# Performance work log

Hardware: AMD Instinct MI355X
Metric: run time of the kernel (lower is better)

## Reference

```python
import jax, jax.numpy as jnp
import numpy as np

B, N_IN, N_HID, N_OUT = 1024, 1024, 2048, 32000


def setup_inputs() -> dict:
    key = jax.random.key(0)
    ks = jax.random.split(key, 9)
    s = lambda fan_in: 1.0 / np.sqrt(fan_in)
    return {
        "input": jax.random.normal(ks[0], (B, N_IN), jnp.float32),
        "hidden": jax.random.normal(ks[1], (B, N_HID), jnp.float32),
        "W_i2g": jax.random.normal(ks[2], (2 * N_HID, N_IN + N_HID), jnp.float32) * s(N_IN + N_HID),
        "b_i2g": jax.random.normal(ks[3], (2 * N_HID,), jnp.float32) * s(N_IN + N_HID),
        "W_x2h": jax.random.normal(ks[4], (N_HID, N_IN), jnp.float32) * s(N_IN),
        "b_x2h": jax.random.normal(ks[5], (N_HID,), jnp.float32) * s(N_IN),
        "W_h2h": jax.random.normal(ks[6], (N_HID, N_HID), jnp.float32) * s(N_HID),
        "W_h2o": jax.random.normal(ks[7], (N_OUT, N_HID), jnp.float32) * s(N_HID),
        "b_h2o": jax.random.normal(ks[8], (N_OUT,), jnp.float32) * s(N_HID),
    }


def reference(input, hidden, W_i2g, b_i2g, W_x2h, b_x2h, W_h2h, W_h2o, b_h2o):
    # combined = cat([input, hidden], dim=1); gates = sigmoid(i2g(combined))
    combined = jnp.concatenate([input, hidden], axis=1)           # [B, n_in+n_hid]
    gates = jax.nn.sigmoid(combined @ W_i2g.T + b_i2g)            # [B, 2*n_hid]
    z, r = gates[:, :N_HID], gates[:, N_HID:]
    # candidate h: tanh(x2h(x) + h2h(r*h)); GRU blend
    h_cand = jnp.tanh(input @ W_x2h.T + b_x2h + (r * hidden) @ W_h2h.T)
    h = z * hidden + (1.0 - z) * h_cand                           # [B, n_hid]
    # dropout in eval mode = identity; h2o + log_softmax over dim 1
    logits = h @ W_h2o.T + b_h2o                                  # [B, n_out]
    output = jax.nn.log_softmax(logits, axis=1)
    return (output, h)
```

## Files before the change

kernel.cpp:

```cpp
#include <hip/hip_runtime.h>
#include <hip/hip_bf16.h>
#include <stdint.h>

using bf16 = __hip_bfloat16;
typedef __bf16 bf16x8 __attribute__((ext_vector_type(8)));
typedef float f32x4 __attribute__((ext_vector_type(4)));

__device__ __forceinline__ void gload_lds16(const bf16* g, bf16* l) {
  __builtin_amdgcn_global_load_lds(
      (const __attribute__((address_space(1))) void*)g,
      (__attribute__((address_space(3))) void*)l, 16, 0, 0);
}

#define BARRIER() asm volatile("s_barrier" ::: "memory")

struct CvtArgs {
  const float* src[5];
  bf16* dst[5];
  int n[5];
  int bstart[6];
};

__global__ __launch_bounds__(256) void cvt_all(CvtArgs a) {
  int seg = 0;
#pragma unroll
  for (int i = 0; i < 4; ++i)
    if ((int)blockIdx.x >= a.bstart[i + 1]) seg = i + 1;
  const int nb = a.bstart[seg + 1] - a.bstart[seg];
  const int lb = blockIdx.x - a.bstart[seg];
  const float* __restrict__ in = a.src[seg];
  bf16* __restrict__ out = a.dst[seg];
  const int n = a.n[seg];
  const int stride = nb * 256 * 4;
  for (int i = (lb * 256 + (int)threadIdx.x) * 4; i < n; i += stride) {
    float4 v = *reinterpret_cast<const float4*>(in + i);
    union { bf16 h[4]; uint2 u; } o;
    o.h[0] = __float2bfloat16(v.x);
    o.h[1] = __float2bfloat16(v.y);
    o.h[2] = __float2bfloat16(v.z);
    o.h[3] = __float2bfloat16(v.w);
    *reinterpret_cast<uint2*>(out + i) = o.u;
  }
}

template <int EPI>
__global__ __launch_bounds__(256)
void gemm128(const bf16* __restrict__ A0, const bf16* __restrict__ A1,
             int aSplit, int ldA0, int ldA1,
             const bf16* __restrict__ B0, const bf16* __restrict__ B1,
             int bSplit, int ldB0, int ldB1,
             int MB, int N, int K,
             const float* __restrict__ bias,
             const float* __restrict__ hidden,
             const bf16* __restrict__ zbuf,
             bf16* __restrict__ obf_a,
             bf16* __restrict__ obf_b,
             float* __restrict__ of32,
             int gemmBlocks,
             const float* __restrict__ csrc,
             bf16* __restrict__ cdst, int cn) {
  const int tid = threadIdx.x;
  if ((int)blockIdx.x >= gemmBlocks) {
    const int cb = blockIdx.x - gemmBlocks;
    const int ncb = gridDim.x - gemmBlocks;
    const int stride = ncb * 256 * 4;
    for (int i = (cb * 256 + tid) * 4; i < cn; i += stride) {
      float4 v = *reinterpret_cast<const float4*>(csrc + i);
      union { bf16 h[4]; uint2 u; } o;
      o.h[0] = __float2bfloat16(v.x);
      o.h[1] = __float2bfloat16(v.y);
      o.h[2] = __float2bfloat16(v.z);
      o.h[3] = __float2bfloat16(v.w);
      *reinterpret_cast<uint2*>(cdst + i) = o.u;
    }
    return;
  }
  __shared__ bf16 lA[2][128 * 64];
  __shared__ bf16 lB[2][128 * 64];
  const int wave = tid >> 6;
  const int lane = tid & 63;
  const int cpx = gemmBlocks >> 3;
  const int swz = ((int)blockIdx.x & 7) * cpx + ((int)blockIdx.x >> 3);
  const int bm = swz % MB;
  const int bn = swz / MB;
  const int wr = wave >> 1, wc = wave & 1;
  const int l8 = lane >> 3;
  const int gcol = ((lane & 7) ^ l8) * 8;
  const int lrow = lane & 15;
  const int kb0 = (lane >> 4) * 16;
  const int xm = (lane & 7) << 4;
  const int nkt = K >> 6;

  auto STAGEK = [&](int buf, int kt) {
    if (kt >= nkt) return;
    const int kb = kt << 6;
    const bf16* Ap; int lda, ka;
    if (kb < aSplit) { Ap = A0; lda = ldA0; ka = kb; }
    else             { Ap = A1; lda = ldA1; ka = kb - aSplit; }
    const bf16* Bp; int ldb, kbb;
    if (kb < bSplit) { Bp = B0; ldb = ldB0; kbb = kb; }
    else             { Bp = B1; ldb = ldB1; kbb = kb - bSplit; }
#pragma unroll
    for (int h = 0; h < 2; ++h)
#pragma unroll
      for (int j = 0; j < 2; ++j) {
        const int r0 = h * 64 + wave * 16 + j * 8;
        gload_lds16(Ap + (size_t)(bm * 128 + r0 + l8) * lda + ka + gcol,
                    &lA[buf][r0 * 64]);
        gload_lds16(Bp + (size_t)(bn * 128 + r0 + l8) * ldb + kbb + gcol,
                    &lB[buf][r0 * 64]);
      }
  };
  auto RDA = [&](int buf, int row, int ks) {
    return *reinterpret_cast<const bf16x8*>(
        reinterpret_cast<const char*>(&lA[buf][0]) + row * 128 +
        ((ks * 64 + kb0) ^ xm));
  };
  auto RDB = [&](int buf, int row, int ks) {
    return *reinterpret_cast<const bf16x8*>(
        reinterpret_cast<const char*>(&lB[buf][0]) + row * 128 +
        ((ks * 64 + kb0) ^ xm));
  };

  f32x4 acc[4][4] = {};

  STAGEK(0, 0);
  asm volatile("s_waitcnt vmcnt(0)" ::: "memory");
  BARRIER();

  for (int kt = 0; kt < nkt; ++kt) {
    const int buf = kt & 1;
    STAGEK(buf ^ 1, kt + 1);
    bf16x8 af[4][2], bfr[4][2];
#pragma unroll
    for (int f = 0; f < 4; ++f)
#pragma unroll
      for (int ks = 0; ks < 2; ++ks) {
        af[f][ks] = RDA(buf, wr * 64 + f * 16 + lrow, ks);
        bfr[f][ks] = RDB(buf, wc * 64 + f * 16 + lrow, ks);
      }
    __builtin_amdgcn_s_setprio(1);
#pragma unroll
    for (int fm = 0; fm < 4; ++fm)
#pragma unroll
      for (int fn = 0; fn < 4; ++fn)
#pragma unroll
        for (int ks = 0; ks < 2; ++ks)
          acc[fm][fn] = __builtin_amdgcn_mfma_f32_16x16x32_bf16(
              af[fm][ks], bfr[fn][ks], acc[fm][fn], 0, 0, 0);
    __builtin_amdgcn_s_setprio(0);
    asm volatile("s_waitcnt vmcnt(0)" ::: "memory");
    BARRIER();
  }

  const int rb = bm * 128 + wr * 64 + (lane >> 4) * 4;
  const int cb = bn * 128 + wc * 64 + lrow;
#pragma unroll
  for (int fm = 0; fm < 4; ++fm) {
#pragma unroll
    for (int fn = 0; fn < 4; ++fn) {
#pragma unroll
      for (int j = 0; j < 4; ++j) {
        const int m = rb + fm * 16 + j;
        const int n = cb + fn * 16;
        float v = acc[fm][fn][j];
        if (EPI == 1) {
          v = 1.0f / (1.0f + __expf(-(v + bias[n])));
          if (n < 2048) {
            obf_a[(size_t)m * 2048 + n] = __float2bfloat16(v);
          } else {
            const int nn = n - 2048;
            obf_b[(size_t)m * 2048 + nn] =
                __float2bfloat16(v * hidden[(size_t)m * 2048 + nn]);
          }
        } else if (EPI == 2) {
          const float e = __expf(2.0f * (v + bias[n]));
          const float hc = (e - 1.0f) / (e + 1.0f);
          const float z = __bfloat162float(zbuf[(size_t)m * 2048 + n]);
          const float hd = hidden[(size_t)m * 2048 + n];
          const float h = z * hd + (1.0f - z) * hc;
          of32[(size_t)m * 2048 + n] = h;
          obf_a[(size_t)m * 2048 + n] = __float2bfloat16(h);
        }
      }
    }
  }
}

__global__ __launch_bounds__(512, 2)
void gemm256_f(const bf16* __restrict__ A, const bf16* __restrict__ W,
               const float* __restrict__ bias, uint32_t* __restrict__ lgt,
               float2* __restrict__ partials, int MB, int K, int NPB) {
  __shared__ bf16 lds[5][256 * 64];
  const int tid = threadIdx.x;
  const int w = tid >> 6, lane = tid & 63;
  const int nwg = gridDim.x;
  const int q8 = nwg >> 3, r8 = nwg & 7;
  const int xcd = (int)blockIdx.x & 7, lid = (int)blockIdx.x >> 3;
  const int swz =
      (xcd < r8 ? xcd * (q8 + 1) : r8 * (q8 + 1) + (xcd - r8) * q8) + lid;
  const int bm = swz % MB, bn = swz / MB;
  const int wr = w >> 2, wc = w & 3;
  const int l8 = lane >> 3;
  const int gcol = ((lane & 7) ^ l8) * 8;
  const int rA = lane & 15;
  const int kb0 = (lane >> 4) * 16;
  const int xm = (lane & 7) << 4;
  const int nkt = K >> 6, niter = nkt >> 1;
  const bf16* gA = A + (size_t)bm * 256 * K;
  const bf16* gB = W + (size_t)bn * 256 * K;

  auto STAGE2 = [&](int plane, int kt, const bf16* g) {
    if (kt > nkt - 1) kt = nkt - 1;
#pragma unroll
    for (int h = 0; h < 2; ++h) {
      const int r0 = h * 128 + w * 16;
#pragma unroll
      for (int j = 0; j < 2; ++j)
        gload_lds16(g + (size_t)(r0 + j * 8 + l8) * K + kt * 64 + gcol,
                    &lds[plane][(r0 + j * 8) * 64]);
    }
  };
  auto RD = [&](int plane, int row, int ks) {
    const int off = row * 128 + ((ks * 64 + kb0) ^ xm);
    return *reinterpret_cast<const bf16x8*>(
        reinterpret_cast<const char*>(&lds[plane][0]) + off);
  };

  f32x4 acc[8][4] = {};

  int a0 = 0, a1 = 1, a2 = 2;
  STAGE2(a0, 0, gA); STAGE2(3, 0, gB);
  STAGE2(a1, 1, gA); STAGE2(4, 1, gB);
  asm volatile("s_waitcnt vmcnt(8)" ::: "memory");
  BARRIER();

  for (int it = 0; it < niter; ++it) {
    const int t = it << 1;
    const bool last = (it == niter - 1);
    bf16x8 bfr[4][2];
#pragma unroll
    for (int ph = 0; ph < 8; ++ph) {
      const int buf = ph >> 2, q = ph & 3;
      const int ap = buf ? a1 : a0;
      const int bp = 3 + buf;
      bf16x8 af[2][2];
      if (q == 0) {
#pragma unroll
        for (int n = 0; n < 4; ++n)
#pragma unroll
          for (int ks = 0; ks < 2; ++ks)
            bfr[n][ks] = RD(bp, wc * 64 + n * 16 + rA, ks);
      }
#pragma unroll
      for (int mm = 0; mm < 2; ++mm)
#pragma unroll
        for (int ks = 0; ks < 2; ++ks)
          af[mm][ks] = RD(ap, wr * 128 + (q * 2 + mm) * 16 + rA, ks);

      if (ph == 1)      STAGE2(a2, t + 2, gA);
      else if (ph == 2) STAGE2(3, t + 2, gB);
      else if (ph == 5) STAGE2(a0, t + 3, gA);
      else if (ph == 6) STAGE2(4, t + 3, gB);

      if (ph == 3 || ph == 7)
        asm volatile("s_waitcnt vmcnt(8)" ::: "memory");
      if (!(ph == 7 && last)) BARRIER();
      __builtin_amdgcn_sched_barrier(0);

      __builtin_amdgcn_s_setprio(1);
#pragma unroll
      for (int mm = 0; mm < 2; ++mm)
#pragma unroll
        for (int n = 0; n < 4; ++n)
#pragma unroll
          for (int ks = 0; ks < 2; ++ks)
            acc[q * 2 + mm][n] = __builtin_amdgcn_mfma_f32_16x16x32_bf16(
                af[mm][ks], bfr[n][ks], acc[q * 2 + mm][n], 0, 0, 0);
      __builtin_amdgcn_s_setprio(0);
    }
    const int na0 = a2, na1 = a0, na2 = a1;
    a0 = na0; a1 = na1; a2 = na2;
  }
  asm volatile("s_waitcnt vmcnt(0) lgkmcnt(0)" ::: "memory");
  __syncthreads();

  float* red = (float*)&lds[0][0];
  float* red2 = red + 1024;
  const int outc = bn * 256 + wc * 64 + rA;
  float bb[4];
#pragma unroll
  for (int n = 0; n < 4; ++n) bb[n] = bias[outc + n * 16];
#pragma unroll
  for (int m = 0; m < 8; ++m)
#pragma unroll
    for (int n = 0; n < 4; ++n)
#pragma unroll
      for (int j = 0; j < 4; ++j) acc[m][n][j] += bb[n];

  const int q4 = lane >> 4;
  const int rowb = wr * 128 + q4 * 4;
#pragma unroll
  for (int m = 0; m < 8; ++m)
#pragma unroll
    for (int j = 0; j < 4; ++j) {
      float x = fmaxf(fmaxf(acc[m][0][j], acc[m][1][j]),
                      fmaxf(acc[m][2][j], acc[m][3][j]));
      x = fmaxf(x, __shfl_xor(x, 1));
      x = fmaxf(x, __shfl_xor(x, 2));
      x = fmaxf(x, __shfl_xor(x, 4));
      x = fmaxf(x, __shfl_xor(x, 8));
      if (rA == 0) red[wc * 256 + rowb + m * 16 + j] = x;
    }
  __syncthreads();
  if (tid < 256)
    red2[tid] = fmaxf(fmaxf(red[0 * 256 + tid], red[1 * 256 + tid]),
                      fmaxf(red[2 * 256 + tid], red[3 * 256 + tid]));
  __syncthreads();

  uint32_t* lgtb = lgt + (size_t)(bm * NPB + bn) * (64 * 512) + tid;
#pragma unroll
  for (int m = 0; m < 8; ++m) {
    const int r0 = rowb + m * 16;
    float s[4];
#pragma unroll
    for (int j = 0; j < 4; ++j) {
      const float fm = red2[r0 + j];
      float e = __expf(acc[m][0][j] - fm) + __expf(acc[m][1][j] - fm) +
                __expf(acc[m][2][j] - fm) + __expf(acc[m][3][j] - fm);
      e += __shfl_xor(e, 1);
      e += __shfl_xor(e, 2);
      e += __shfl_xor(e, 4);
      e += __shfl_xor(e, 8);
      s[j] = e;
    }
#pragma unroll
    for (int j = 0; j < 4; ++j)
      if (rA == 0) red[wc * 256 + r0 + j] = s[j];
#pragma unroll
    for (int n = 0; n < 4; ++n)
#pragma unroll
      for (int k = 0; k < 2; ++k) {
        union { bf16 h[2]; uint32_t u; } pk;
        pk.h[0] = __float2bfloat16(acc[m][n][2 * k]);
        pk.h[1] = __float2bfloat16(acc[m][n][2 * k + 1]);
        lgtb[(size_t)(m * 8 + n * 2 + k) * 512] = pk.u;
      }
  }
  __syncthreads();
  if (tid < 256) {
    const float ssum = red[0 * 256 + tid] + red[1 * 256 + tid] +
                       red[2 * 256 + tid] + red[3 * 256 + tid];
    partials[(size_t)(bm * 256 + tid) * NPB + bn] =
        make_float2(red2[tid], ssum);
  }
}

__global__ __launch_bounds__(128) void lse_reduce(
    const float2* __restrict__ partials, float* __restrict__ lse, int NPB) {
  const int row = blockIdx.x;
  const int t = threadIdx.x;
  float m = -3.4e38f, s = 0.0f;
  if (t < NPB) {
    float2 p = partials[(size_t)row * NPB + t];
    m = p.x;
    s = p.y;
  }
#pragma unroll
  for (int o = 32; o; o >>= 1) {
    const float om = __shfl_xor(m, o), os = __shfl_xor(s, o);
    const float nm = fmaxf(m, om);
    s = s * __expf(m - nm) + os * __expf(om - nm);
    m = nm;
  }
  __shared__ float sm[2], ss[2];
  if ((t & 63) == 0) { sm[t >> 6] = m; ss[t >> 6] = s; }
  __syncthreads();
  if (t == 0) {
    const float M = fmaxf(sm[0], sm[1]);
    const float S = ss[0] * __expf(sm[0] - M) + ss[1] * __expf(sm[1] - M);
    lse[row] = M + __logf(S);
  }
}

__global__ __launch_bounds__(512) void ls_final(
    const uint32_t* __restrict__ lgt, const float* __restrict__ lse,
    float* __restrict__ out, int NPB) {
  const int blk = blockIdx.x;
  const int bm = blk / NPB, bn = blk % NPB;
  const int t = threadIdx.x;
  const int w = t >> 6, lane = t & 63;
  const int wr = w >> 2, wc = w & 3, q4 = lane >> 4, rAc = lane & 15;
  const uint32_t* src = lgt + (size_t)blk * (64 * 512) + t;
  const int col = bn * 256 + wc * 64 + rAc;
  const int row0 = bm * 256 + wr * 128 + q4 * 4;
#pragma unroll 4
  for (int fp = 0; fp < 64; ++fp) {
    const int m = fp >> 3, n = (fp >> 1) & 3, k = fp & 1;
    const uint32_t u = src[(size_t)fp * 512];
    const int r = row0 + m * 16 + 2 * k;
    const int c = col + n * 16;
    const float lo = __uint_as_float(u << 16);
    const float hi = __uint_as_float(u & 0xffff0000u);
    out[(size_t)r * 32000 + c] = lo - lse[r];
    out[(size_t)(r + 1) * 32000 + c] = hi - lse[r + 1];
  }
}

extern "C" void kernel_launch(void* const* d_in, const int* in_sizes, int n_in,
                              void* d_out, int out_size, void* d_ws,
                              size_t ws_size, hipStream_t stream) {
  const float* input  = (const float*)d_in[0];
  const float* hidden = (const float*)d_in[1];
  const float* W_i2g  = (const float*)d_in[2];
  const float* b_i2g  = (const float*)d_in[3];
  const float* W_x2h  = (const float*)d_in[4];
  const float* b_x2h  = (const float*)d_in[5];
  const float* W_h2h  = (const float*)d_in[6];
  const float* W_h2o  = (const float*)d_in[7];
  const float* b_h2o  = (const float*)d_in[8];

  float* out_ls = (float*)d_out;
  float* out_h  = out_ls + (size_t)1024 * 32000;

  char* ws = (char*)d_ws;
  bf16* inp_bf     = (bf16*)(ws + 0);
  bf16* hid_bf     = (bf16*)(ws + 2097152);
  bf16* wi_bf      = (bf16*)(ws + 6291456);
  bf16* wx_bf      = (bf16*)(ws + 31457280);
  bf16* wh_bf      = (bf16*)(ws + 35651584);
  bf16* z_bf       = (bf16*)(ws + 44040192);
  bf16* rh_bf      = (bf16*)(ws + 48234496);
  bf16* h_bf       = (bf16*)(ws + 52428800);
  bf16* wo_bf      = (bf16*)(ws + 56623104);
  uint32_t* lgt    = (uint32_t*)(ws + 187695104);
  float2* partials = (float2*)(ws + 253231104);
  float* lse       = (float*)(ws + 254255104);

  CvtArgs ca;
  ca.src[0] = input;  ca.dst[0] = inp_bf; ca.n[0] = 1024 * 1024;
  ca.src[1] = hidden; ca.dst[1] = hid_bf; ca.n[1] = 1024 * 2048;
  ca.src[2] = W_i2g;  ca.dst[2] = wi_bf;  ca.n[2] = 4096 * 3072;
  ca.src[3] = W_x2h;  ca.dst[3] = wx_bf;  ca.n[3] = 2048 * 1024;
  ca.src[4] = W_h2h;  ca.dst[4] = wh_bf;  ca.n[4] = 2048 * 2048;
  const int bs[6] = {0, 24, 72, 370, 418, 512};
  for (int i = 0; i < 6; ++i) ca.bstart[i] = bs[i];
  cvt_all<<<512, 256, 0, stream>>>(ca);

  const int HALF_WO = 32000 * 2048 / 2;

  gemm128<1><<<256 + 256, 256, 0, stream>>>(
      inp_bf, hid_bf, 1024, 1024, 2048,
      wi_bf, wi_bf, 1 << 30, 3072, 3072,
      8, 4096, 3072, b_i2g, hidden, nullptr, z_bf, rh_bf, nullptr,
      256, W_h2o, wo_bf, HALF_WO);

  gemm128<2><<<128 + 384, 256, 0, stream>>>(
      inp_bf, rh_bf, 1024, 1024, 2048,
      wx_bf, wh_bf, 1024, 1024, 2048,
      8, 2048, 3072, b_x2h, hidden, z_bf, h_bf, nullptr, out_h,
      128, W_h2o + HALF_WO, wo_bf + HALF_WO, HALF_WO);

  gemm256_f<<<4 * 125, 512, 0, stream>>>(h_bf, wo_bf, b_h2o, lgt, partials,
                                         4, 2048, 125);

  lse_reduce<<<1024, 128, 0, stream>>>(partials, lse, 125);
  ls_final<<<500, 512, 0, stream>>>(lgt, lse, out_ls, 125);
}
```

Baseline: 368.8 us.

## Fuse fp32-to-bf16 conversion into GEMM staging and merge LSE reduce into final pass

Removes the separate conversion kernel. The two gate and candidate GEMMs now load fp32 activations and weights through registers and convert them to bf16 while writing LDS. The W_h2o conversion work is rebalanced: part of it runs in dedicated blocks and the rest runs in the GEMM blocks after their epilogue. The separate lse_reduce kernel is folded into ls_final, which recomputes each row's log-sum-exp in shared memory. This saves launches and the bf16 round trip through memory, but gives up async global-to-LDS loads for register staging, doubles the global bytes read per tile, and recomputes the LSE once per column block.

```diff
diff --git a/kernel.cpp b/kernel.cpp
--- a/kernel.cpp
+++ b/kernel.cpp
@@ -14,42 +14,23 @@
 
 #define BARRIER() asm volatile("s_barrier" ::: "memory")
 
-struct CvtArgs {
-  const float* src[5];
-  bf16* dst[5];
-  int n[5];
-  int bstart[6];
-};
-
-__global__ __launch_bounds__(256) void cvt_all(CvtArgs a) {
-  int seg = 0;
-#pragma unroll
-  for (int i = 0; i < 4; ++i)
-    if ((int)blockIdx.x >= a.bstart[i + 1]) seg = i + 1;
-  const int nb = a.bstart[seg + 1] - a.bstart[seg];
-  const int lb = blockIdx.x - a.bstart[seg];
-  const float* __restrict__ in = a.src[seg];
-  bf16* __restrict__ out = a.dst[seg];
-  const int n = a.n[seg];
-  const int stride = nb * 256 * 4;
-  for (int i = (lb * 256 + (int)threadIdx.x) * 4; i < n; i += stride) {
-    float4 v = *reinterpret_cast<const float4*>(in + i);
-    union { bf16 h[4]; uint2 u; } o;
-    o.h[0] = __float2bfloat16(v.x);
-    o.h[1] = __float2bfloat16(v.y);
-    o.h[2] = __float2bfloat16(v.z);
-    o.h[3] = __float2bfloat16(v.w);
-    *reinterpret_cast<uint2*>(out + i) = o.u;
-  }
-}
-
-template <int EPI>
+__device__ __forceinline__ uint4 cvt8(float4 a, float4 b) {
+  union { bf16 h[8]; uint4 q; } u;
+  u.h[0] = __float2bfloat16(a.x); u.h[1] = __float2bfloat16(a.y);
+  u.h[2] = __float2bfloat16(a.z); u.h[3] = __float2bfloat16(a.w);
+  u.h[4] = __float2bfloat16(b.x); u.h[5] = __float2bfloat16(b.y);
+  u.h[6] = __float2bfloat16(b.z); u.h[7] = __float2bfloat16(b.w);
+  return u.q;
+}
+
+template <int EPI, int A1BF>
 __global__ __launch_bounds__(256)
-void gemm128(const bf16* __restrict__ A0, const bf16* __restrict__ A1,
+void gemm128(const float* __restrict__ A0f, const float* __restrict__ A1f,
+             const bf16* __restrict__ A1h,
              int aSplit, int ldA0, int ldA1,
-             const bf16* __restrict__ B0, const bf16* __restrict__ B1,
+             const float* __restrict__ B0f, const float* __restrict__ B1f,
              int bSplit, int ldB0, int ldB1,
-             int MB, int N, int K,
+             int MB, int K,
              const float* __restrict__ bias,
              const float* __restrict__ hidden,
              const bf16* __restrict__ zbuf,
@@ -58,19 +39,17 @@
              float* __restrict__ of32,
              int gemmBlocks,
              const float* __restrict__ csrc,
-             bf16* __restrict__ cdst, int cn) {
+             bf16* __restrict__ cdst, int cn, int cvtSplit) {
   const int tid = threadIdx.x;
   if ((int)blockIdx.x >= gemmBlocks) {
     const int cb = blockIdx.x - gemmBlocks;
     const int ncb = gridDim.x - gemmBlocks;
     const int stride = ncb * 256 * 4;
-    for (int i = (cb * 256 + tid) * 4; i < cn; i += stride) {
+    for (int i = (cb * 256 + tid) * 4; i < cvtSplit; i += stride) {
       float4 v = *reinterpret_cast<const float4*>(csrc + i);
       union { bf16 h[4]; uint2 u; } o;
-      o.h[0] = __float2bfloat16(v.x);
-      o.h[1] = __float2bfloat16(v.y);
-      o.h[2] = __float2bfloat16(v.z);
-      o.h[3] = __float2bfloat16(v.w);
+      o.h[0] = __float2bfloat16(v.x); o.h[1] = __float2bfloat16(v.y);
+      o.h[2] = __float2bfloat16(v.z); o.h[3] = __float2bfloat16(v.w);
       *reinterpret_cast<uint2*>(cdst + i) = o.u;
     }
     return;
@@ -84,32 +63,73 @@
   const int bm = swz % MB;
   const int bn = swz / MB;
   const int wr = wave >> 1, wc = wave & 1;
-  const int l8 = lane >> 3;
-  const int gcol = ((lane & 7) ^ l8) * 8;
   const int lrow = lane & 15;
   const int kb0 = (lane >> 4) * 16;
   const int xm = (lane & 7) << 4;
   const int nkt = K >> 6;
-
-  auto STAGEK = [&](int buf, int kt) {
+  const int rS = tid >> 3;
+  const int l8b = tid & 7;
+
+  float4 ra[4][2], rb[4][2];
+
+  auto STAGE_A = [&](int buf, int kt) {
     if (kt >= nkt) return;
     const int kb = kt << 6;
-    const bf16* Ap; int lda, ka;
-    if (kb < aSplit) { Ap = A0; lda = ldA0; ka = kb; }
-    else             { Ap = A1; lda = ldA1; ka = kb - aSplit; }
-    const bf16* Bp; int ldb, kbb;
-    if (kb < bSplit) { Bp = B0; ldb = ldB0; kbb = kb; }
-    else             { Bp = B1; ldb = ldB1; kbb = kb - bSplit; }
-#pragma unroll
-    for (int h = 0; h < 2; ++h)
-#pragma unroll
-      for (int j = 0; j < 2; ++j) {
-        const int r0 = h * 64 + wave * 16 + j * 8;
-        gload_lds16(Ap + (size_t)(bm * 128 + r0 + l8) * lda + ka + gcol,
-                    &lA[buf][r0 * 64]);
-        gload_lds16(Bp + (size_t)(bn * 128 + r0 + l8) * ldb + kbb + gcol,
-                    &lB[buf][r0 * 64]);
+    const bool seg1 = (kb >= aSplit);
+    const int kloc = seg1 ? kb - aSplit : kb;
+    const int ld = seg1 ? ldA1 : ldA0;
+#pragma unroll
+    for (int p = 0; p < 4; ++p) {
+      const int r = p * 32 + rS;
+      const int c8 = (l8b ^ (r & 7)) * 8;
+      if (A1BF && seg1) {
+        gload_lds16(A1h + (size_t)(bm * 128 + r) * ld + kloc + c8,
+                    &lA[buf][(p * 32 + wave * 8) * 64]);
+      } else {
+        const float* s = (seg1 ? A1f : A0f) +
+                         (size_t)(bm * 128 + r) * ld + kloc + c8;
+        ra[p][0] = *reinterpret_cast<const float4*>(s);
+        ra[p][1] = *reinterpret_cast<const float4*>(s + 4);
       }
+    }
+  };
+  auto WRITE_A = [&](int buf, int kt) {
+    if (kt >= nkt) return;
+    const int kb = kt << 6;
+    if (A1BF && kb >= aSplit) return;
+#pragma unroll
+    for (int p = 0; p < 4; ++p) {
+      const int r = p * 32 + rS;
+      *reinterpret_cast<uint4*>(
+          reinterpret_cast<char*>(&lA[buf][0]) + r * 128 + l8b * 16) =
+          cvt8(ra[p][0], ra[p][1]);
+    }
+  };
+  auto STAGE_B = [&](int kt) {
+    if (kt >= nkt) return;
+    const int kb = kt << 6;
+    const bool seg1 = (kb >= bSplit);
+    const int kloc = seg1 ? kb - bSplit : kb;
+    const int ld = seg1 ? ldB1 : ldB0;
+    const float* base = seg1 ? B1f : B0f;
+#pragma unroll
+    for (int p = 0; p < 4; ++p) {
+      const int r = p * 32 + rS;
+      const int c8 = (l8b ^ (r & 7)) * 8;
+      const float* s = base + (size_t)(bn * 128 + r) * ld + kloc + c8;
+      rb[p][0] = *reinterpret_cast<const float4*>(s);
+      rb[p][1] = *reinterpret_cast<const float4*>(s + 4);
+    }
+  };
+  auto WRITE_B = [&](int buf, int kt) {
+    if (kt >= nkt) return;
+#pragma unroll
+    for (int p = 0; p < 4; ++p) {
+      const int r = p * 32 + rS;
+      *reinterpret_cast<uint4*>(
+          reinterpret_cast<char*>(&lB[buf][0]) + r * 128 + l8b * 16) =
+          cvt8(rb[p][0], rb[p][1]);
+    }
   };
   auto RDA = [&](int buf, int row, int ks) {
     return *reinterpret_cast<const bf16x8*>(
@@ -124,13 +144,14 @@
 
   f32x4 acc[4][4] = {};
 
-  STAGEK(0, 0);
-  asm volatile("s_waitcnt vmcnt(0)" ::: "memory");
-  BARRIER();
+  STAGE_A(0, 0); STAGE_B(0);
+  WRITE_A(0, 0); WRITE_B(0, 0);
+  __syncthreads();
 
   for (int kt = 0; kt < nkt; ++kt) {
     const int buf = kt & 1;
-    STAGEK(buf ^ 1, kt + 1);
+    STAGE_A(buf ^ 1, kt + 1);
+    STAGE_B(kt + 1);
     bf16x8 af[4][2], bfr[4][2];
 #pragma unroll
     for (int f = 0; f < 4; ++f)
@@ -149,20 +170,21 @@
           acc[fm][fn] = __builtin_amdgcn_mfma_f32_16x16x32_bf16(
               af[fm][ks], bfr[fn][ks], acc[fm][fn], 0, 0, 0);
     __builtin_amdgcn_s_setprio(0);
-    asm volatile("s_waitcnt vmcnt(0)" ::: "memory");
-    BARRIER();
-  }
-
-  const int rb = bm * 128 + wr * 64 + (lane >> 4) * 4;
-  const int cb = bn * 128 + wc * 64 + lrow;
+    WRITE_A(buf ^ 1, kt + 1);
+    WRITE_B(buf ^ 1, kt + 1);
+    __syncthreads();
+  }
+
+  const int rb_ = bm * 128 + wr * 64 + (lane >> 4) * 4;
+  const int cb_ = bn * 128 + wc * 64 + lrow;
 #pragma unroll
   for (int fm = 0; fm < 4; ++fm) {
 #pragma unroll
     for (int fn = 0; fn < 4; ++fn) {
 #pragma unroll
       for (int j = 0; j < 4; ++j) {
-        const int m = rb + fm * 16 + j;
-        const int n = cb + fn * 16;
+        const int m = rb_ + fm * 16 + j;
+        const int n = cb_ + fn * 16;
         float v = acc[fm][fn][j];
         if (EPI == 1) {
           v = 1.0f / (1.0f + __expf(-(v + bias[n])));
@@ -183,6 +205,18 @@
           obf_a[(size_t)m * 2048 + n] = __float2bfloat16(h);
         }
       }
+    }
+  }
+
+  {
+    const int stride = gemmBlocks * 256 * 4;
+    for (int i = cvtSplit + ((int)blockIdx.x * 256 + tid) * 4; i < cn;
+         i += stride) {
+      float4 v = *reinterpret_cast<const float4*>(csrc + i);
+      union { bf16 h[4]; uint2 u; } o;
+      o.h[0] = __float2bfloat16(v.x); o.h[1] = __float2bfloat16(v.y);
+      o.h[2] = __float2bfloat16(v.z); o.h[3] = __float2bfloat16(v.w);
+      *reinterpret_cast<uint2*>(cdst + i) = o.u;
     }
   }
 }
@@ -356,54 +390,49 @@
   }
 }
 
-__global__ __launch_bounds__(128) void lse_reduce(
-    const float2* __restrict__ partials, float* __restrict__ lse, int NPB) {
-  const int row = blockIdx.x;
+__global__ __launch_bounds__(512) void ls_final(
+    const uint32_t* __restrict__ lgt, const float2* __restrict__ partials,
+    float* __restrict__ out, int NPB) {
+  __shared__ float lse_s[256];
+  const int blk = blockIdx.x;
+  const int bm = blk / NPB, bn = blk % NPB;
   const int t = threadIdx.x;
-  float m = -3.4e38f, s = 0.0f;
-  if (t < NPB) {
-    float2 p = partials[(size_t)row * NPB + t];
-    m = p.x;
-    s = p.y;
-  }
-#pragma unroll
-  for (int o = 32; o; o >>= 1) {
-    const float om = __shfl_xor(m, o), os = __shfl_xor(s, o);
+  {
+    const int row = t >> 1, half = t & 1;
+    const int lo = half ? 63 : 0;
+    const int hi = half ? NPB : 63;
+    float m = -3.4e38f, s = 0.0f;
+    const float2* pp = partials + (size_t)(bm * 256 + row) * NPB;
+    for (int i = lo; i < hi; ++i) {
+      const float2 p = pp[i];
+      const float nm = fmaxf(m, p.x);
+      s = s * __expf(m - nm) + p.y * __expf(p.x - nm);
+      m = nm;
+    }
+    const float om = __shfl_xor(m, 1), os = __shfl_xor(s, 1);
     const float nm = fmaxf(m, om);
     s = s * __expf(m - nm) + os * __expf(om - nm);
     m = nm;
-  }
-  __shared__ float sm[2], ss[2];
-  if ((t & 63) == 0) { sm[t >> 6] = m; ss[t >> 6] = s; }
-  __syncthreads();
-  if (t == 0) {
-    const float M = fmaxf(sm[0], sm[1]);
-    const float S = ss[0] * __expf(sm[0] - M) + ss[1] * __expf(sm[1] - M);
-    lse[row] = M + __logf(S);
-  }
-}
-
-__global__ __launch_bounds__(512) void ls_final(
-    const uint32_t* __restrict__ lgt, const float* __restrict__ lse,
-    float* __restrict__ out, int NPB) {
-  const int blk = blockIdx.x;
-  const int bm = blk / NPB, bn = blk % NPB;
-  const int t = threadIdx.x;
+    if (half == 0) lse_s[row] = m + __logf(s);
+  }
+  __syncthreads();
+
   const int w = t >> 6, lane = t & 63;
   const int wr = w >> 2, wc = w & 3, q4 = lane >> 4, rAc = lane & 15;
   const uint32_t* src = lgt + (size_t)blk * (64 * 512) + t;
   const int col = bn * 256 + wc * 64 + rAc;
-  const int row0 = bm * 256 + wr * 128 + q4 * 4;
+  const int row0g = bm * 256;
+  const int row0l = wr * 128 + q4 * 4;
 #pragma unroll 4
   for (int fp = 0; fp < 64; ++fp) {
     const int m = fp >> 3, n = (fp >> 1) & 3, k = fp & 1;
     const uint32_t u = src[(size_t)fp * 512];
-    const int r = row0 + m * 16 + 2 * k;
+    const int rl = row0l + m * 16 + 2 * k;
     const int c = col + n * 16;
     const float lo = __uint_as_float(u << 16);
     const float hi = __uint_as_float(u & 0xffff0000u);
-    out[(size_t)r * 32000 + c] = lo - lse[r];
-    out[(size_t)(r + 1) * 32000 + c] = hi - lse[r + 1];
+    out[(size_t)(row0g + rl) * 32000 + c] = lo - lse_s[rl];
+    out[(size_t)(row0g + rl + 1) * 32000 + c] = hi - lse_s[rl + 1];
   }
 }
 
@@ -424,46 +453,29 @@
   float* out_h  = out_ls + (size_t)1024 * 32000;
 
   char* ws = (char*)d_ws;
-  bf16* inp_bf     = (bf16*)(ws + 0);
-  bf16* hid_bf     = (bf16*)(ws + 2097152);
-  bf16* wi_bf      = (bf16*)(ws + 6291456);
-  bf16* wx_bf      = (bf16*)(ws + 31457280);
-  bf16* wh_bf      = (bf16*)(ws + 35651584);
-  bf16* z_bf       = (bf16*)(ws + 44040192);
-  bf16* rh_bf      = (bf16*)(ws + 48234496);
-  bf16* h_bf       = (bf16*)(ws + 52428800);
-  bf16* wo_bf      = (bf16*)(ws + 56623104);
-  uint32_t* lgt    = (uint32_t*)(ws + 187695104);
-  float2* partials = (float2*)(ws + 253231104);
-  float* lse       = (float*)(ws + 254255104);
-
-  CvtArgs ca;
-  ca.src[0] = input;  ca.dst[0] = inp_bf; ca.n[0] = 1024 * 1024;
-  ca.src[1] = hidden; ca.dst[1] = hid_bf; ca.n[1] = 1024 * 2048;
-  ca.src[2] = W_i2g;  ca.dst[2] = wi_bf;  ca.n[2] = 4096 * 3072;
-  ca.src[3] = W_x2h;  ca.dst[3] = wx_bf;  ca.n[3] = 2048 * 1024;
-  ca.src[4] = W_h2h;  ca.dst[4] = wh_bf;  ca.n[4] = 2048 * 2048;
-  const int bs[6] = {0, 24, 72, 370, 418, 512};
-  for (int i = 0; i < 6; ++i) ca.bstart[i] = bs[i];
-  cvt_all<<<512, 256, 0, stream>>>(ca);
+  bf16* z_bf       = (bf16*)(ws + 0);
+  bf16* rh_bf      = (bf16*)(ws + 4194304);
+  bf16* h_bf       = (bf16*)(ws + 8388608);
+  bf16* wo_bf      = (bf16*)(ws + 12582912);
+  uint32_t* lgt    = (uint32_t*)(ws + 143654912);
+  float2* partials = (float2*)(ws + 210763776);
 
   const int HALF_WO = 32000 * 2048 / 2;
 
-  gemm128<1><<<256 + 256, 256, 0, stream>>>(
-      inp_bf, hid_bf, 1024, 1024, 2048,
-      wi_bf, wi_bf, 1 << 30, 3072, 3072,
-      8, 4096, 3072, b_i2g, hidden, nullptr, z_bf, rh_bf, nullptr,
-      256, W_h2o, wo_bf, HALF_WO);
-
-  gemm128<2><<<128 + 384, 256, 0, stream>>>(
-      inp_bf, rh_bf, 1024, 1024, 2048,
-      wx_bf, wh_bf, 1024, 1024, 2048,
-      8, 2048, 3072, b_x2h, hidden, z_bf, h_bf, nullptr, out_h,
-      128, W_h2o + HALF_WO, wo_bf + HALF_WO, HALF_WO);
+  gemm128<1, 0><<<512, 256, 0, stream>>>(
+      input, hidden, nullptr, 1024, 1024, 2048,
+      W_i2g, W_i2g, 1 << 30, 3072, 3072,
+      8, 3072, b_i2g, hidden, nullptr, z_bf, rh_bf, nullptr,
+      256, W_h2o, wo_bf, HALF_WO, 20480000);
+
+  gemm128<2, 1><<<512, 256, 0, stream>>>(
+      input, nullptr, rh_bf, 1024, 1024, 2048,
+      W_x2h, W_h2h, 1024, 1024, 2048,
+      8, 3072, b_x2h, hidden, z_bf, h_bf, nullptr, out_h,
+      128, W_h2o + HALF_WO, wo_bf + HALF_WO, HALF_WO, 24576000);
 
   gemm256_f<<<4 * 125, 512, 0, stream>>>(h_bf, wo_bf, b_h2o, lgt, partials,
                                          4, 2048, 125);
 
-  lse_reduce<<<1024, 128, 0, stream>>>(partials, lse, 125);
-  ls_final<<<500, 512, 0, stream>>>(lgt, lse, out_ls, 125);
-}
+  ls_final<<<500, 512, 0, stream>>>(lgt, partials, out_ls, 125);
+}
```

Measured after the change: 602.9 us. +63.5%, slower.
